# Performance work log

Measured on AMD Instinct MI355X. Metric: run time of the kernel, lower is better.

Reference implementation:

```python
import jax, jax.numpy as jnp
import numpy as np

B, V = 256, 128000

def setup_inputs() -> dict:
    key = jax.random.key(0)
    k1, k2 = jax.random.split(key)
    logits = jax.random.normal(k1, (B, V), dtype=jnp.float32)
    temperatures = jax.random.uniform(k2, (B,), dtype=jnp.float32)
    return {"logits": logits, "temperatures": temperatures}

def reference(logits, temperatures):
    # temperature-scaled probs (float32), temp==0 treated as 1 for the divide
    logits_f = logits.astype(jnp.float32)
    safe_t = jnp.where(temperatures == 0, jnp.ones_like(temperatures), temperatures)
    scaled = logits_f / safe_t[:, None]                      # [B, V]
    probs = jax.nn.softmax(scaled, axis=-1)                  # [B, V] fp32
    # greedy tokens from the ORIGINAL logits (torch in-place div only touched the copy)
    greedy_tokens = jnp.argmax(logits_f, axis=-1)            # [B] int
    # multinomial sampling == Gumbel-max / categorical over scaled logits
    sample_key = jax.random.key(42)
    sampled_tokens = jax.random.categorical(sample_key, scaled, axis=-1)  # [B]
    tokens = jnp.where(temperatures == 0, greedy_tokens, sampled_tokens)
    return tokens, probs
```

## Files before the change

### kernel.cpp

```cpp
#include <hip/hip_runtime.h>
#include <cstdint>
#include <cmath>

#define B_ROWS 256
#define V_COLS 128000
#define CHUNKS 25
#define CHUNK_QUADS 1280
#define ATHREADS 256
#define AWAVES 4
#define QPT 5
#define LN2F 0.69314718055994530942f
#define GUMBEL_WINDOW 21.2f

#define G_STRIDE 4
#define FIN_OFF (B_ROWS * CHUNKS * G_STRIDE)
#define S_OFF (FIN_OFF + B_ROWS * 4)

__device__ __forceinline__ uint32_t rotl32(uint32_t x, uint32_t d) {
  return __builtin_amdgcn_alignbit(x, x, 32u - d);
}

__device__ __forceinline__ uint32_t threefry_xor_pre(uint32_t x1) {
  const uint32_t k1 = 42u;
  const uint32_t k2 = 0x1BD11BF0u;
  uint32_t x0 = 0u;
#define TF_RND(r) { x0 += x1; x1 = rotl32(x1, (r)); x1 ^= x0; }
  TF_RND(13) TF_RND(15) TF_RND(26) TF_RND(6)
  x0 += k1; x1 += k2 + 1u;
  TF_RND(17) TF_RND(29) TF_RND(16) TF_RND(24)
  x0 += k2; x1 += 0u + 2u;
  TF_RND(13) TF_RND(15) TF_RND(26) TF_RND(6)
  x0 += 0u; x1 += k1 + 3u;
  TF_RND(17) TF_RND(29) TF_RND(16) TF_RND(24)
  x0 += k1; x1 += k2 + 4u;
  TF_RND(13) TF_RND(15) TF_RND(26) TF_RND(6)
  x0 += k2; x1 += 0u + 5u;
#undef TF_RND
  return x0 ^ x1;
}

__device__ __forceinline__ float gumbel_ll2(uint32_t bits) {
  uint32_t ub = (bits >> 9) | 0x3f800000u;
  float f = __uint_as_float(ub) - 1.0f;
  float u = fmaxf(f, 1.17549435e-38f);
  return __log2f(-__log2f(u));
}

__global__ __launch_bounds__(ATHREADS) void pass1_kernel(
    const float* __restrict__ logits,
    const float* __restrict__ temps,
    float* __restrict__ ws) {
  const uint32_t bx = blockIdx.x;
  const uint32_t b = bx / CHUNKS;
  const uint32_t chunk = bx - b * CHUNKS;
  const int tid = threadIdx.x;
  const float t = temps[b];
  const float inv_t = (t == 0.0f) ? 1.0f : (1.0f / t);
  const float* __restrict__ row = logits + (size_t)b * V_COLS;
  const int q0 = (int)chunk * CHUNK_QUADS + tid;

  float4 xq[QPT];
#pragma unroll
  for (int j = 0; j < QPT; ++j)
    xq[j] = reinterpret_cast<const float4*>(row)[q0 + j * ATHREADS];

  float av = -INFINITY; int ai = 0;
  const int v0 = q0 * 4;
#pragma unroll
  for (int j = 0; j < QPT; ++j) {
    const float xa[4] = {xq[j].x, xq[j].y, xq[j].z, xq[j].w};
#pragma unroll
    for (int k = 0; k < 4; ++k) {
      const bool up = xa[k] > av;
      av = up ? xa[k] : av;
      ai = up ? (v0 + j * 1024 + k) : ai;
    }
  }

  const float mthr = av * inv_t;
  float s = 0.0f;
#pragma unroll
  for (int j = 0; j < QPT; ++j) {
    s += __expf(fmaf(xq[j].x, inv_t, -mthr));
    s += __expf(fmaf(xq[j].y, inv_t, -mthr));
    s += __expf(fmaf(xq[j].z, inv_t, -mthr));
    s += __expf(fmaf(xq[j].w, inv_t, -mthr));
  }

  float m = mthr;
#pragma unroll
  for (int off = 32; off > 0; off >>= 1) {
    float ov = __shfl_xor(av, off);
    int   oi = __shfl_xor(ai, off);
    if (ov > av || (ov == av && oi < ai)) { av = ov; ai = oi; }
    float om = __shfl_xor(m, off);
    float os = __shfl_xor(s, off);
    float mn = fmaxf(m, om);
    s = fmaf(s, __expf(m - mn), os * __expf(om - mn));
    m = mn;
  }

  __shared__ float lds_av[AWAVES]; __shared__ int lds_ai[AWAVES];
  __shared__ float lds_m[AWAVES];  __shared__ float lds_s[AWAVES];
  const int wid = tid >> 6;
  if ((tid & 63) == 0) {
    lds_av[wid] = av; lds_ai[wid] = ai;
    lds_m[wid] = m;   lds_s[wid] = s;
  }
  __syncthreads();
  if (tid == 0) {
    float Av = lds_av[0]; int Ai = lds_ai[0];
    float M = lds_m[0];   float S = lds_s[0];
#pragma unroll
    for (int w = 1; w < AWAVES; ++w) {
      float ov = lds_av[w]; int oi = lds_ai[w];
      if (ov > Av || (ov == Av && oi < Ai)) { Av = ov; Ai = oi; }
      float om = lds_m[w]; float os = lds_s[w];
      float mn = fmaxf(M, om);
      S = fmaf(S, __expf(M - mn), os * __expf(om - mn));
      M = mn;
    }
    float* p = ws + (size_t)(b * CHUNKS + chunk) * G_STRIDE;
    p[0] = Av; p[1] = __int_as_float(Ai);
    p[2] = M;  p[3] = S;
  }
}

__global__ __launch_bounds__(B_ROWS) void fin1_kernel(
    float* __restrict__ ws) {
  const int r = threadIdx.x;
  const float* p = ws + (size_t)r * CHUNKS * G_STRIDE;
  float Av = -INFINITY; int Ai = 0;
  float M = -INFINITY;  float S = 0.0f;
#pragma unroll
  for (int c = 0; c < CHUNKS; ++c) {
    const float* q = p + c * G_STRIDE;
    float ov = q[0]; int oi = __float_as_int(q[1]);
    if (ov > Av) { Av = ov; Ai = oi; }
    float om = q[2]; float os = q[3];
    float mn = fmaxf(M, om);
    S = fmaf(S, __expf(M - mn), os * __expf(om - mn));
    M = mn;
  }
  float* f = ws + FIN_OFF + 4 * r;
  f[0] = M;
  f[1] = 1.0f / S;
  f[2] = __int_as_float(Ai);
}

__global__ __launch_bounds__(ATHREADS) void pass2_kernel(
    const float* __restrict__ logits,
    const float* __restrict__ temps,
    float* __restrict__ ws,
    float* __restrict__ out) {
  const uint32_t bx = blockIdx.x;
  const uint32_t b = bx / CHUNKS;
  const uint32_t chunk = bx - b * CHUNKS;
  const int tid = threadIdx.x;
  const float t = temps[b];
  const float inv_t = (t == 0.0f) ? 1.0f : (1.0f / t);
  const float M = ws[FIN_OFF + 4 * b + 0];
  const float invS = ws[FIN_OFF + 4 * b + 1];
  const float* __restrict__ row = logits + (size_t)b * V_COLS;
  float* __restrict__ prow = out + B_ROWS + (size_t)b * V_COLS;
  const int q0 = (int)chunk * CHUNK_QUADS + tid;
  const int v0 = q0 * 4;
  const uint32_t cb42 = b * (uint32_t)V_COLS + (uint32_t)v0 + 42u;
  const float thrM = M - GUMBEL_WINDOW;

  float gv = -INFINITY; int gi = 0;

  if (t != 0.0f) {
#pragma unroll
    for (int j = 0; j < QPT; ++j) {
      const float4 x4 = reinterpret_cast<const float4*>(row)[q0 + j * ATHREADS];
      float4 p4;
      p4.x = __expf(fmaf(x4.x, inv_t, -M)) * invS;
      p4.y = __expf(fmaf(x4.y, inv_t, -M)) * invS;
      p4.z = __expf(fmaf(x4.z, inv_t, -M)) * invS;
      p4.w = __expf(fmaf(x4.w, inv_t, -M)) * invS;
      reinterpret_cast<float4*>(prow)[q0 + j * ATHREADS] = p4;
      const float xa[4] = {x4.x, x4.y, x4.z, x4.w};
      const float mx4 = fmaxf(fmaxf(xa[0], xa[1]), fmaxf(xa[2], xa[3]));
      if (__any(mx4 * inv_t > thrM)) {
#pragma unroll
        for (int k = 0; k < 4; ++k) {
          const float sxv = xa[k] * inv_t;
          const float c = fmaf(-LN2F,
              gumbel_ll2(threefry_xor_pre(cb42 + (uint32_t)(j * 1024 + k))),
              sxv);
          const bool up = c > gv;
          gv = up ? c : gv;
          gi = up ? (v0 + j * 1024 + k) : gi;
        }
      }
    }

#pragma unroll
    for (int off = 32; off > 0; off >>= 1) {
      float ov = __shfl_xor(gv, off);
      int   oi = __shfl_xor(gi, off);
      if (ov > gv || (ov == gv && oi < gi)) { gv = ov; gi = oi; }
    }

    __shared__ float lds_gv[AWAVES]; __shared__ int lds_gi[AWAVES];
    const int wid = tid >> 6;
    if ((tid & 63) == 0) { lds_gv[wid] = gv; lds_gi[wid] = gi; }
    __syncthreads();
    if (tid == 0) {
      float Gv = lds_gv[0]; int Gi = lds_gi[0];
#pragma unroll
      for (int w = 1; w < AWAVES; ++w) {
        float ov = lds_gv[w]; int oi = lds_gi[w];
        if (ov > Gv || (ov == Gv && oi < Gi)) { Gv = ov; Gi = oi; }
      }
      float* p = ws + S_OFF + (size_t)(b * CHUNKS + chunk) * 2;
      p[0] = Gv; p[1] = __int_as_float(Gi);
    }
  } else {
#pragma unroll
    for (int j = 0; j < QPT; ++j) {
      const float4 x4 = reinterpret_cast<const float4*>(row)[q0 + j * ATHREADS];
      float4 p4;
      p4.x = __expf(fmaf(x4.x, inv_t, -M)) * invS;
      p4.y = __expf(fmaf(x4.y, inv_t, -M)) * invS;
      p4.z = __expf(fmaf(x4.z, inv_t, -M)) * invS;
      p4.w = __expf(fmaf(x4.w, inv_t, -M)) * invS;
      reinterpret_cast<float4*>(prow)[q0 + j * ATHREADS] = p4;
    }
  }
}

__global__ __launch_bounds__(B_ROWS) void fin2_kernel(
    const float* __restrict__ temps,
    const float* __restrict__ ws,
    float* __restrict__ out) {
  const int r = threadIdx.x;
  const float t = temps[r];
  int token;
  if (t == 0.0f) {
    token = __float_as_int(ws[FIN_OFF + 4 * r + 2]);
  } else {
    const float* p = ws + S_OFF + (size_t)r * CHUNKS * 2;
    float Sv = -INFINITY; int Si = 0;
#pragma unroll
    for (int c = 0; c < CHUNKS; ++c) {
      float ov = p[2 * c]; int oi = __float_as_int(p[2 * c + 1]);
      if (ov > Sv) { Sv = ov; Si = oi; }
    }
    token = Si;
  }
  out[r] = (float)token;
}

extern "C" void kernel_launch(void* const* d_in, const int* in_sizes, int n_in,
                              void* d_out, int out_size, void* d_ws, size_t ws_size,
                              hipStream_t stream) {
  const float* logits = (const float*)d_in[0];
  const float* temps  = (const float*)d_in[1];
  float* out = (float*)d_out;
  float* ws  = (float*)d_ws;
  pass1_kernel<<<B_ROWS * CHUNKS, ATHREADS, 0, stream>>>(logits, temps, ws);
  fin1_kernel<<<1, B_ROWS, 0, stream>>>(ws);
  pass2_kernel<<<B_ROWS * CHUNKS, ATHREADS, 0, stream>>>(logits, temps, ws, out);
  fin2_kernel<<<1, B_ROWS, 0, stream>>>(temps, ws, out);
}
```

Baseline: 102.9 us.

## Fold fin1 reduction into pass2, skip Gumbel for chunks below window, fold invS into exp

Removes the single-block fin1 kernel: each pass2 block recomputes the row's merged max and sum from the 25 chunk partials, and fin2 now computes the greedy argmax itself. Pass2 also skips the Gumbel sampling branch for a whole chunk when that chunk's scaled max lies more than the window below the row max, writing a -inf sentinel instead. The probability multiply by 1/S is folded into the exponent offset. This drops one launch and the serial fin1 step at the cost of redundant per-block partial merges and a small change in rounding.

```diff
diff --git a/kernel.cpp b/kernel.cpp
--- a/kernel.cpp
+++ b/kernel.cpp
@@ -9,12 +9,11 @@
 #define ATHREADS 256
 #define AWAVES 4
 #define QPT 5
-#define LN2F 0.69314718055994530942f
+#define LOG2E 1.4426950408889634f
 #define GUMBEL_WINDOW 21.2f
 
 #define G_STRIDE 4
-#define FIN_OFF (B_ROWS * CHUNKS * G_STRIDE)
-#define S_OFF (FIN_OFF + B_ROWS * 4)
+#define S_OFF (B_ROWS * CHUNKS * G_STRIDE)
 
 __device__ __forceinline__ uint32_t rotl32(uint32_t x, uint32_t d) {
   return __builtin_amdgcn_alignbit(x, x, 32u - d);
@@ -126,28 +125,6 @@
   }
 }
 
-__global__ __launch_bounds__(B_ROWS) void fin1_kernel(
-    float* __restrict__ ws) {
-  const int r = threadIdx.x;
-  const float* p = ws + (size_t)r * CHUNKS * G_STRIDE;
-  float Av = -INFINITY; int Ai = 0;
-  float M = -INFINITY;  float S = 0.0f;
-#pragma unroll
-  for (int c = 0; c < CHUNKS; ++c) {
-    const float* q = p + c * G_STRIDE;
-    float ov = q[0]; int oi = __float_as_int(q[1]);
-    if (ov > Av) { Av = ov; Ai = oi; }
-    float om = q[2]; float os = q[3];
-    float mn = fmaxf(M, om);
-    S = fmaf(S, __expf(M - mn), os * __expf(om - mn));
-    M = mn;
-  }
-  float* f = ws + FIN_OFF + 4 * r;
-  f[0] = M;
-  f[1] = 1.0f / S;
-  f[2] = __int_as_float(Ai);
-}
-
 __global__ __launch_bounds__(ATHREADS) void pass2_kernel(
     const float* __restrict__ logits,
     const float* __restrict__ temps,
@@ -159,36 +136,50 @@
   const int tid = threadIdx.x;
   const float t = temps[b];
   const float inv_t = (t == 0.0f) ? 1.0f : (1.0f / t);
-  const float M = ws[FIN_OFF + 4 * b + 0];
-  const float invS = ws[FIN_OFF + 4 * b + 1];
+
+  const float* gp = ws + (size_t)b * CHUNKS * G_STRIDE;
+  float M = -INFINITY, S = 0.0f;
+#pragma unroll
+  for (int c = 0; c < CHUNKS; ++c) {
+    const float om = gp[c * G_STRIDE + 2];
+    const float os = gp[c * G_STRIDE + 3];
+    const float mn = fmaxf(M, om);
+    S = fmaf(S, __expf(M - mn), os * __expf(om - mn));
+    M = mn;
+  }
+  const float invS = 1.0f / S;
+  const float cexp = __logf(invS) - M;
+  const float a = inv_t * LOG2E;
+  const float myM = gp[chunk * G_STRIDE + 2];
+  const float thrM = M - GUMBEL_WINDOW;
+
   const float* __restrict__ row = logits + (size_t)b * V_COLS;
   float* __restrict__ prow = out + B_ROWS + (size_t)b * V_COLS;
   const int q0 = (int)chunk * CHUNK_QUADS + tid;
   const int v0 = q0 * 4;
   const uint32_t cb42 = b * (uint32_t)V_COLS + (uint32_t)v0 + 42u;
-  const float thrM = M - GUMBEL_WINDOW;
-
-  float gv = -INFINITY; int gi = 0;
-
-  if (t != 0.0f) {
+
+  const bool doG = (t != 0.0f) && (myM > thrM);
+
+  if (doG) {
+    float gv = -INFINITY; int gi = 0;
 #pragma unroll
     for (int j = 0; j < QPT; ++j) {
       const float4 x4 = reinterpret_cast<const float4*>(row)[q0 + j * ATHREADS];
       float4 p4;
-      p4.x = __expf(fmaf(x4.x, inv_t, -M)) * invS;
-      p4.y = __expf(fmaf(x4.y, inv_t, -M)) * invS;
-      p4.z = __expf(fmaf(x4.z, inv_t, -M)) * invS;
-      p4.w = __expf(fmaf(x4.w, inv_t, -M)) * invS;
+      p4.x = __expf(fmaf(x4.x, inv_t, cexp));
+      p4.y = __expf(fmaf(x4.y, inv_t, cexp));
+      p4.z = __expf(fmaf(x4.z, inv_t, cexp));
+      p4.w = __expf(fmaf(x4.w, inv_t, cexp));
       reinterpret_cast<float4*>(prow)[q0 + j * ATHREADS] = p4;
       const float xa[4] = {x4.x, x4.y, x4.z, x4.w};
       const float mx4 = fmaxf(fmaxf(xa[0], xa[1]), fmaxf(xa[2], xa[3]));
       if (__any(mx4 * inv_t > thrM)) {
 #pragma unroll
         for (int k = 0; k < 4; ++k) {
-          const float sxv = xa[k] * inv_t;
-          const float c = fmaf(-LN2F,
-              gumbel_ll2(threefry_xor_pre(cb42 + (uint32_t)(j * 1024 + k))),
-              sxv);
+          const float ll2 =
+              gumbel_ll2(threefry_xor_pre(cb42 + (uint32_t)(j * 1024 + k)));
+          const float c = fmaf(xa[k], a, -ll2);
           const bool up = c > gv;
           gv = up ? c : gv;
           gi = up ? (v0 + j * 1024 + k) : gi;
@@ -222,11 +213,15 @@
     for (int j = 0; j < QPT; ++j) {
       const float4 x4 = reinterpret_cast<const float4*>(row)[q0 + j * ATHREADS];
       float4 p4;
-      p4.x = __expf(fmaf(x4.x, inv_t, -M)) * invS;
-      p4.y = __expf(fmaf(x4.y, inv_t, -M)) * invS;
-      p4.z = __expf(fmaf(x4.z, inv_t, -M)) * invS;
-      p4.w = __expf(fmaf(x4.w, inv_t, -M)) * invS;
+      p4.x = __expf(fmaf(x4.x, inv_t, cexp));
+      p4.y = __expf(fmaf(x4.y, inv_t, cexp));
+      p4.z = __expf(fmaf(x4.z, inv_t, cexp));
+      p4.w = __expf(fmaf(x4.w, inv_t, cexp));
       reinterpret_cast<float4*>(prow)[q0 + j * ATHREADS] = p4;
+    }
+    if (t != 0.0f && tid == 0) {
+      float* p = ws + S_OFF + (size_t)(b * CHUNKS + chunk) * 2;
+      p[0] = -INFINITY; p[1] = __int_as_float(0);
     }
   }
 }
@@ -239,13 +234,20 @@
   const float t = temps[r];
   int token;
   if (t == 0.0f) {
-    token = __float_as_int(ws[FIN_OFF + 4 * r + 2]);
+    const float* gp = ws + (size_t)r * CHUNKS * G_STRIDE;
+    float Av = -INFINITY; int Ai = 0;
+#pragma unroll
+    for (int c = 0; c < CHUNKS; ++c) {
+      float ov = gp[c * G_STRIDE]; int oi = __float_as_int(gp[c * G_STRIDE + 1]);
+      if (ov > Av) { Av = ov; Ai = oi; }
+    }
+    token = Ai;
   } else {
-    const float* p = ws + S_OFF + (size_t)r * CHUNKS * 2;
+    const float* sp = ws + S_OFF + (size_t)r * CHUNKS * 2;
     float Sv = -INFINITY; int Si = 0;
 #pragma unroll
     for (int c = 0; c < CHUNKS; ++c) {
-      float ov = p[2 * c]; int oi = __float_as_int(p[2 * c + 1]);
+      float ov = sp[2 * c]; int oi = __float_as_int(sp[2 * c + 1]);
       if (ov > Sv) { Sv = ov; Si = oi; }
     }
     token = Si;
@@ -261,7 +263,6 @@
   float* out = (float*)d_out;
   float* ws  = (float*)d_ws;
   pass1_kernel<<<B_ROWS * CHUNKS, ATHREADS, 0, stream>>>(logits, temps, ws);
-  fin1_kernel<<<1, B_ROWS, 0, stream>>>(ws);
   pass2_kernel<<<B_ROWS * CHUNKS, ATHREADS, 0, stream>>>(logits, temps, ws, out);
   fin2_kernel<<<1, B_ROWS, 0, stream>>>(temps, ws, out);
 }
```

After: 110.0 us. 6.9% more time.
